# Performance work log

Measured on AMD Instinct MI355X. Metric: run time of the kernel, lower is better.

The kernel has to match this reference:

```python
import jax, jax.numpy as jnp
import numpy as np

B, D, T, K = 16, 256, 1024, 8192
BETA = 0.25
EPS = 1e-10


def setup_inputs() -> dict:
    key = jax.random.key(0)
    k1, k2 = jax.random.split(key)
    z = jax.random.normal(k1, (B, D, T), dtype=jnp.float32)
    # codebook initialized uniform(-1/K, 1/K) like the torch module
    embedding = jax.random.uniform(k2, (K, D), dtype=jnp.float32,
                                   minval=-1.0 / K, maxval=1.0 / K)
    return {"z": z, "embedding": embedding}


def reference(z, embedding):
    # z: [B, D, T] -> [B, T, D]
    zf = jnp.transpose(z, (0, 2, 1))
    # squared L2 distances to each codebook entry: [B, T, K]
    d = (jnp.sum(zf ** 2, axis=2, keepdims=True)
         + jnp.sum(embedding ** 2, axis=1)
         - 2.0 * jnp.einsum('btd,kd->btk', zf, embedding))
    idx = jnp.argmin(d, axis=2)                         # [B, T] int
    min_encodings = jax.nn.one_hot(idx, K, dtype=jnp.float32)  # [B, T, K]
    z_q = embedding[idx]                                # [B, T, D]
    z_q = jnp.transpose(z_q, (0, 2, 1))                 # [B, D, T]

    codebook_loss = jnp.mean((z - jax.lax.stop_gradient(z_q)) ** 2)
    commitment_loss = jnp.mean((jax.lax.stop_gradient(z) - z_q) ** 2)
    vq_loss = codebook_loss + BETA * commitment_loss

    # perplexity exactly as in torch code: mean over dim 0 only -> [T, K]
    avg_probs = jnp.mean(min_encodings, axis=0)
    perplexity = jnp.exp(-jnp.sum(avg_probs * jnp.log(avg_probs + EPS)))

    return z_q, vq_loss, perplexity, idx
```

## Files before the change

kernel.cpp:

```cpp
#include <hip/hip_runtime.h>
#include <hip/hip_bf16.h>
#include <float.h>
#include <math.h>

#define NB 16
#define ND 256
#define NT 1024
#define NK 8192
#define NBT (NB*NT)
#define PTS 64
#define KCH 512
#define DROWS 16
#define NSTG ((NK/KCH)*(ND/DROWS))

typedef float f32x2 __attribute__((ext_vector_type(2)));


__global__ void k_ssq(const float* __restrict__ emb, float* __restrict__ ssq,
                      double* __restrict__ loss_sum, double* __restrict__ ent_sum) {
    int k = blockIdx.x * 4 + (threadIdx.x >> 6);
    int lane = threadIdx.x & 63;
    float4 v = *reinterpret_cast<const float4*>(emb + (size_t)k * ND + lane * 4);
    float s = v.x * v.x + v.y * v.y + v.z * v.z + v.w * v.w;
#pragma unroll
    for (int off = 32; off; off >>= 1) s += __shfl_down(s, off, 64);
    if (lane == 0) ssq[k] = s;
    if (blockIdx.x == 0 && threadIdx.x == 0) { *loss_sum = 0.0; *ent_sum = 0.0; }
}

__global__ __launch_bounds__(256)
void k_tr(const float* __restrict__ emb, float* __restrict__ embT) {
    __shared__ float T[64][65];
    const int kt = blockIdx.x >> 2, dt = blockIdx.x & 3;
    const int k0 = kt * 64, d0 = dt * 64;
    const int r = threadIdx.x >> 4;
    const int c4 = (threadIdx.x & 15) * 4;
#pragma unroll
    for (int j = 0; j < 4; ++j) {
        int kk = r + 16 * j;
        float4 v = *reinterpret_cast<const float4*>(emb + (size_t)(k0 + kk) * ND + d0 + c4);
        T[kk][c4 + 0] = v.x; T[kk][c4 + 1] = v.y; T[kk][c4 + 2] = v.z; T[kk][c4 + 3] = v.w;
    }
    __syncthreads();
#pragma unroll
    for (int j = 0; j < 4; ++j) {
        int dr = r + 16 * j;
        float4 w = {T[c4 + 0][dr], T[c4 + 1][dr], T[c4 + 2][dr], T[c4 + 3][dr]};
        *reinterpret_cast<float4*>(embT + (size_t)(d0 + dr) * NK + k0 + c4) = w;
    }
}

__device__ __forceinline__ void dd_fma(f32x2 (&acc2)[8][4],
                                       float4 e0, float4 e1, float4 z0, float4 z1) {
    f32x2 e01 = {e0.x, e0.y}, e23 = {e0.z, e0.w};
    f32x2 e45 = {e1.x, e1.y}, e67 = {e1.z, e1.w};
    float zs[8] = {z0.x, z0.y, z0.z, z0.w, z1.x, z1.y, z1.z, z1.w};
#pragma unroll
    for (int p = 0; p < 8; ++p) {
        f32x2 zp2 = {zs[p], zs[p]};
        acc2[p][0] = __builtin_elementwise_fma(zp2, e01, acc2[p][0]);
        acc2[p][1] = __builtin_elementwise_fma(zp2, e23, acc2[p][1]);
        acc2[p][2] = __builtin_elementwise_fma(zp2, e45, acc2[p][2]);
        acc2[p][3] = __builtin_elementwise_fma(zp2, e67, acc2[p][3]);
    }
}

__global__ __launch_bounds__(512)
void k_main(const float* __restrict__ z, const float* __restrict__ embT,
            const float* __restrict__ ssq, int* __restrict__ idx_out,
            float* __restrict__ idxf_out) {
    __shared__ float Zs[ND][PTS];
    __shared__ float As[PTS];
    __shared__ float Es[2][DROWS][KCH];
    float* redD = &Es[0][0][0];
    int*   redK = reinterpret_cast<int*>(&Es[0][0][0]) + 64 * 65;

    const int tid = threadIdx.x;
    const int b  = blockIdx.x >> 4;
    const int t0 = (blockIdx.x & 15) * PTS;
    const int py = tid >> 6;
    const int kx = tid & 63;

    auto issue_stage = [&](int s, int buf) {
        const int kc2 = s >> 4, dh2 = s & 15;
        const float* gb = embT + (size_t)(dh2 * DROWS + 2 * py) * NK + kc2 * KCH + kx * 4;
#pragma unroll
        for (int j = 0; j < 2; ++j)
#pragma unroll
            for (int hf = 0; hf < 2; ++hf)
                __builtin_amdgcn_global_load_lds(
                    (const __attribute__((address_space(1))) void*)(gb + (size_t)j * NK + hf * 256),
                    (__attribute__((address_space(3))) void*)(&Es[buf][2 * py + j][hf * 256]),
                    16, 0, 0);
    };

    issue_stage(0, 0);

    const float* zb = z + ((size_t)b * ND) * NT + t0;
#pragma unroll
    for (int it = 0; it < 8; ++it) {
        int i4 = (it * 512 + tid) * 4;
        int d = i4 >> 6, i = i4 & 63;
        *reinterpret_cast<float4*>(&Zs[d][i]) =
            *reinterpret_cast<const float4*>(zb + (size_t)d * NT + i);
    }
    __syncthreads();

    if (tid < PTS) {
        float a = 0.f;
        for (int d = 0; d < ND; ++d) {
            float x = Zs[d][tid];
            a = __fadd_rn(a, __fmul_rn(x, x));
        }
        As[tid] = a;
    }

    float best[8]; int bk[8];
#pragma unroll
    for (int p = 0; p < 8; ++p) { best[p] = FLT_MAX; bk[p] = 0; }

    for (int kc = 0; kc < NK / KCH; ++kc) {
        f32x2 acc2[8][4];
#pragma unroll
        for (int p = 0; p < 8; ++p)
#pragma unroll
            for (int j = 0; j < 4; ++j) acc2[p][j] = (f32x2){0.f, 0.f};

        for (int dh = 0; dh < ND / DROWS; ++dh) {
            const int s  = kc * (ND / DROWS) + dh;
            const int cb = s & 1;
            if (s + 1 < NSTG) issue_stage(s + 1, cb ^ 1);

            const float* e0b = &Es[cb][0][kx * 4];
            const float* e1b = &Es[cb][0][256 + kx * 4];
            const float* zr  = &Zs[dh * DROWS][py * 8];
#pragma unroll
            for (int d2 = 0; d2 < DROWS / 2; ++d2) {
                const int da = 2 * d2, db2 = 2 * d2 + 1;
                float4 ae0 = *reinterpret_cast<const float4*>(e0b + da * KCH);
                float4 ae1 = *reinterpret_cast<const float4*>(e1b + da * KCH);
                float4 az0 = *reinterpret_cast<const float4*>(zr + da * PTS);
                float4 az1 = *reinterpret_cast<const float4*>(zr + da * PTS + 4);
                float4 be0 = *reinterpret_cast<const float4*>(e0b + db2 * KCH);
                float4 be1 = *reinterpret_cast<const float4*>(e1b + db2 * KCH);
                float4 bz0 = *reinterpret_cast<const float4*>(zr + db2 * PTS);
                float4 bz1 = *reinterpret_cast<const float4*>(zr + db2 * PTS + 4);
                dd_fma(acc2, ae0, ae1, az0, az1);
                dd_fma(acc2, be0, be1, bz0, bz1);
                __builtin_amdgcn_sched_barrier(0);
            }
            __syncthreads();
        }
        const float* sq = ssq + kc * KCH;
        float4 s0 = *reinterpret_cast<const float4*>(sq + kx * 4);
        float4 s1 = *reinterpret_cast<const float4*>(sq + 256 + kx * 4);
        float sqv[8] = {s0.x, s0.y, s0.z, s0.w, s1.x, s1.y, s1.z, s1.w};
#pragma unroll
        for (int p = 0; p < 8; ++p) {
            float A = As[py * 8 + p];
#pragma unroll
            for (int q = 0; q < 8; ++q) {
                float cq = (q & 1) ? acc2[p][q >> 1].y : acc2[p][q >> 1].x;
                float s = __fadd_rn(A, sqv[q]);
                float dist = __fsub_rn(s, 2.0f * cq);
                if (dist < best[p]) {
                    best[p] = dist;
                    bk[p] = kc * KCH + (q < 4 ? kx * 4 + q : 256 + kx * 4 + (q - 4));
                }
            }
        }
    }
    __syncthreads();
#pragma unroll
    for (int p = 0; p < 8; ++p) {
        redD[(py * 8 + p) * 65 + kx] = best[p];
        redK[(py * 8 + p) * 65 + kx] = bk[p];
    }
    __syncthreads();
    if (tid < PTS) {
        float bd = redD[tid * 65]; int bb = redK[tid * 65];
        for (int x = 1; x < 64; ++x) {
            float dx = redD[tid * 65 + x]; int kk2 = redK[tid * 65 + x];
            if (dx < bd || (dx == bd && kk2 < bb)) { bd = dx; bb = kk2; }
        }
        int pg = b * NT + t0 + tid;
        idx_out[pg] = bb;
        idxf_out[pg] = (float)bb;
    }
}

__global__ __launch_bounds__(256)
void k_zq(const float* __restrict__ z, const float* __restrict__ emb,
          const int* __restrict__ idx, float* __restrict__ zq,
          double* __restrict__ loss_sum) {
    __shared__ int bkS[PTS];
    __shared__ double wred[4];
    const int bid = blockIdx.x;
    const int b = bid >> 4, t0 = (bid & 15) * PTS;
    const int tid = threadIdx.x;
    if (tid < PTS) bkS[tid] = idx[b * NT + t0 + tid];
    __syncthreads();
    const int i = tid & 63, dq = tid >> 6;
    const float* erow = emb + (size_t)bkS[i] * ND;
    double ls = 0.0;
    for (int j = 0; j < 64; ++j) {
        int d = dq * 64 + j;
        float qv = erow[d];
        float zv = z[((size_t)b * ND + d) * NT + t0 + i];
        float df = __fsub_rn(zv, qv);
        ls = fma((double)df, (double)df, ls);
        zq[((size_t)b * ND + d) * NT + t0 + i] = qv;
    }
#pragma unroll
    for (int off = 32; off; off >>= 1) ls += __shfl_down(ls, off, 64);
    if ((tid & 63) == 0) wred[tid >> 6] = ls;
    __syncthreads();
    if (tid == 0) atomicAdd(loss_sum, wred[0] + wred[1] + wred[2] + wred[3]);
}

__global__ void k_ent(const int* __restrict__ idx, double* __restrict__ ent_sum) {
    __shared__ double wred[4];
    int t = blockIdx.x * 256 + threadIdx.x;
    int v[16];
#pragma unroll
    for (int i = 0; i < NB; ++i) v[i] = idx[i * NT + t];
    double s = 0.0;
#pragma unroll
    for (int i = 0; i < NB; ++i) {
        bool first = true;
        for (int j = 0; j < i; ++j) if (v[j] == v[i]) first = false;
        if (first) {
            int c = 1;
            for (int j = i + 1; j < NB; ++j) c += (v[j] == v[i]);
            float p = (float)c * 0.0625f;
            s += (double)(p * logf(p + 1e-10f));
        }
    }
#pragma unroll
    for (int off = 32; off; off >>= 1) s += __shfl_down(s, off, 64);
    if ((threadIdx.x & 63) == 0) wred[threadIdx.x >> 6] = s;
    __syncthreads();
    if (threadIdx.x == 0) {
        double tot = wred[0] + wred[1] + wred[2] + wred[3];
        atomicAdd(ent_sum, tot);
    }
}

__global__ void k_fin(const double* __restrict__ loss_sum,
                      const double* __restrict__ ent_sum, float* __restrict__ out) {
    if (threadIdx.x == 0 && blockIdx.x == 0) {
        float L = (float)(*loss_sum / (double)(NB * ND * NT));
        out[4194304] = __fadd_rn(L, 0.25f * L);
        float S = (float)(-*ent_sum);
        out[4194305] = expf(fminf(S, 87.0f));
    }
}

extern "C" void kernel_launch(void* const* d_in, const int* in_sizes, int n_in,
                              void* d_out, int out_size, void* d_ws, size_t ws_size,
                              hipStream_t stream) {
    const float* z   = (const float*)d_in[0];
    const float* emb = (const float*)d_in[1];
    float* out = (float*)d_out;

    float*  ssq      = (float*)d_ws;
    int*    idx      = (int*)((char*)d_ws + 32768);
    double* loss_sum = (double*)((char*)d_ws + 98304);
    double* ent_sum  = (double*)((char*)d_ws + 98312);

    float* zq   = out;
    float* embT = out;
    float* idxf = out + 4194306;

    k_ssq<<<NK / 4, 256, 0, stream>>>(emb, ssq, loss_sum, ent_sum);
    k_tr<<<(NK / 64) * (ND / 64), 256, 0, stream>>>(emb, embT);
    k_main<<<NBT / PTS, 512, 0, stream>>>(z, embT, ssq, idx, idxf);
    k_zq<<<NBT / PTS, 256, 0, stream>>>(z, emb, idx, zq, loss_sum);
    k_ent<<<NT / 256, 256, 0, stream>>>(idx, ent_sum);
    k_fin<<<1, 64, 0, stream>>>(loss_sum, ent_sum, out);
}
```

Measured before the change: 812.0 us.

## Stream z rows from global memory via wave-uniform scalar loads instead of LDS tile

New measurement: 873.8 us. 7.6% more time.

```diff
diff --git a/kernel.cpp b/kernel.cpp
--- a/kernel.cpp
+++ b/kernel.cpp
@@ -69,9 +69,8 @@
 void k_main(const float* __restrict__ z, const float* __restrict__ embT,
             const float* __restrict__ ssq, int* __restrict__ idx_out,
             float* __restrict__ idxf_out) {
-    __shared__ float Zs[ND][PTS];
+    __shared__ float Es[2][DROWS][KCH];
     __shared__ float As[PTS];
-    __shared__ float Es[2][DROWS][KCH];
     float* redD = &Es[0][0][0];
     int*   redK = reinterpret_cast<int*>(&Es[0][0][0]) + 64 * 65;
 
@@ -96,28 +95,29 @@
 
     issue_stage(0, 0);
 
-    const float* zb = z + ((size_t)b * ND) * NT + t0;
-#pragma unroll
-    for (int it = 0; it < 8; ++it) {
-        int i4 = (it * 512 + tid) * 4;
-        int d = i4 >> 6, i = i4 & 63;
-        *reinterpret_cast<float4*>(&Zs[d][i]) =
-            *reinterpret_cast<const float4*>(zb + (size_t)d * NT + i);
-    }
-    __syncthreads();
-
     if (tid < PTS) {
+        const float* zp = z + ((size_t)b * ND) * NT + t0 + tid;
         float a = 0.f;
         for (int d = 0; d < ND; ++d) {
-            float x = Zs[d][tid];
+            float x = zp[(size_t)d * NT];
             a = __fadd_rn(a, __fmul_rn(x, x));
         }
         As[tid] = a;
     }
 
+    const int wpy = __builtin_amdgcn_readfirstlane(py);
+    const float* zw = z + ((size_t)b * ND) * NT + t0 + wpy * 8;
+
+    __syncthreads();
+
     float best[8]; int bk[8];
 #pragma unroll
     for (int p = 0; p < 8; ++p) { best[p] = FLT_MAX; bk[p] = 0; }
+
+    float4 cz0 = *reinterpret_cast<const float4*>(zw);
+    float4 cz1 = *reinterpret_cast<const float4*>(zw + 4);
+    float4 cz2 = *reinterpret_cast<const float4*>(zw + NT);
+    float4 cz3 = *reinterpret_cast<const float4*>(zw + NT + 4);
 
     for (int kc = 0; kc < NK / KCH; ++kc) {
         f32x2 acc2[8][4];
@@ -133,21 +133,23 @@
 
             const float* e0b = &Es[cb][0][kx * 4];
             const float* e1b = &Es[cb][0][256 + kx * 4];
-            const float* zr  = &Zs[dh * DROWS][py * 8];
-#pragma unroll
-            for (int d2 = 0; d2 < DROWS / 2; ++d2) {
+#pragma unroll
+            for (int d2 = 0; d2 < 8; ++d2) {
                 const int da = 2 * d2, db2 = 2 * d2 + 1;
+                const int dn = ((dh * DROWS + da) + 2) & 255;
+                const float* zn = zw + (size_t)dn * NT;
+                float4 nz0 = *reinterpret_cast<const float4*>(zn);
+                float4 nz1 = *reinterpret_cast<const float4*>(zn + 4);
+                float4 nz2 = *reinterpret_cast<const float4*>(zn + NT);
+                float4 nz3 = *reinterpret_cast<const float4*>(zn + NT + 4);
                 float4 ae0 = *reinterpret_cast<const float4*>(e0b + da * KCH);
                 float4 ae1 = *reinterpret_cast<const float4*>(e1b + da * KCH);
-                float4 az0 = *reinterpret_cast<const float4*>(zr + da * PTS);
-                float4 az1 = *reinterpret_cast<const float4*>(zr + da * PTS + 4);
                 float4 be0 = *reinterpret_cast<const float4*>(e0b + db2 * KCH);
                 float4 be1 = *reinterpret_cast<const float4*>(e1b + db2 * KCH);
-                float4 bz0 = *reinterpret_cast<const float4*>(zr + db2 * PTS);
-                float4 bz1 = *reinterpret_cast<const float4*>(zr + db2 * PTS + 4);
-                dd_fma(acc2, ae0, ae1, az0, az1);
-                dd_fma(acc2, be0, be1, bz0, bz1);
+                dd_fma(acc2, ae0, ae1, cz0, cz1);
+                dd_fma(acc2, be0, be1, cz2, cz3);
                 __builtin_amdgcn_sched_barrier(0);
+                cz0 = nz0; cz1 = nz1; cz2 = nz2; cz3 = nz3;
             }
             __syncthreads();
         }
```
